# Optimization experiments

Hardware: AMD Instinct MI355X
Metric: run time of the kernel (lower is better)

Reference implementation:

```python
import jax, jax.numpy as jnp
import numpy as np

N_NODES = 100000
N_EDGES = 1000000
N_GRAPHS = 1024
F_IN = 128
N_CLASSES = 10
BN_EPS = 1e-5


def _lin(key, fan_in, fan_out):
    k1, k2 = jax.random.split(key)
    b = 1.0 / np.sqrt(fan_in)
    W = jax.random.uniform(k1, (fan_out, fan_in), minval=-b, maxval=b, dtype=jnp.float32)
    bias = jax.random.uniform(k2, (fan_out,), minval=-b, maxval=b, dtype=jnp.float32)
    return W, bias


def setup_inputs() -> dict:
    key = jax.random.key(0)
    ks = jax.random.split(key, 16)
    inp = {
        "atom_feats": jax.random.normal(ks[0], (N_NODES, F_IN), dtype=jnp.float32),
        "edge_src": jax.random.randint(ks[1], (N_EDGES,), 0, N_NODES),
        "edge_dst": jax.random.randint(ks[2], (N_EDGES,), 0, N_NODES),
        "graph_ids": jnp.sort(jax.random.randint(ks[3], (N_NODES,), 0, N_GRAPHS)),
    }
    # conv1: F_IN -> 32 with batch-norm on edge features
    inp["Wt1"], inp["bt1"] = _lin(ks[4], F_IN, 32)
    inp["Wp1"], inp["bp1"] = _lin(ks[5], F_IN, 32)
    inp["bn_gamma"] = jnp.ones((32,), jnp.float32)
    inp["bn_beta"] = jnp.zeros((32,), jnp.float32)
    inp["bn_mean"] = jnp.zeros((32,), jnp.float32)
    inp["bn_var"] = jnp.ones((32,), jnp.float32)
    # conv2: 32 -> 64 ; conv3: 64 -> 64
    inp["Wt2"], inp["bt2"] = _lin(ks[6], 32, 64)
    inp["Wp2"], inp["bp2"] = _lin(ks[7], 32, 64)
    inp["Wt3"], inp["bt3"] = _lin(ks[8], 64, 64)
    inp["Wp3"], inp["bp3"] = _lin(ks[9], 64, 64)
    # fc layers
    inp["Wf1"], inp["bf1"] = _lin(ks[10], 64, 64)
    inp["Wf2"], inp["bf2"] = _lin(ks[11], 64, 32)
    inp["Wf3"], inp["bf3"] = _lin(ks[12], 32, N_CLASSES)
    return inp


def _seg_max(vals, ids, n):
    m = jax.ops.segment_max(vals, ids, num_segments=n)
    return jnp.where(jnp.isfinite(m), m, 0.0)  # zero-in-degree -> 0 (DGL semantics)


def _edgeconv(x, src, dst, Wt, bt, Wp, bp, bn=None):
    xs = x[src]                      # [E, f_in] gather src
    xd = x[dst]                      # [E, f_in] gather dst
    e = (xd - xs) @ Wt.T + bt + (xs @ Wp.T + bp)  # [E, f_out]
    if bn is not None:
        gamma, beta, mean, var = bn
        e = (e - mean) * (gamma / jnp.sqrt(var + BN_EPS)) + beta
    return _seg_max(e, dst, x.shape[0])


def reference(atom_feats, edge_src, edge_dst, graph_ids,
              Wt1, bt1, Wp1, bp1, bn_gamma, bn_beta, bn_mean, bn_var,
              Wt2, bt2, Wp2, bp2, Wt3, bt3, Wp3, bp3,
              Wf1, bf1, Wf2, bf2, Wf3, bf3):
    x = jax.nn.elu(_edgeconv(atom_feats, edge_src, edge_dst, Wt1, bt1, Wp1, bp1,
                             bn=(bn_gamma, bn_beta, bn_mean, bn_var)))
    x = jax.nn.elu(_edgeconv(x, edge_src, edge_dst, Wt2, bt2, Wp2, bp2))
    x = jax.nn.elu(_edgeconv(x, edge_src, edge_dst, Wt3, bt3, Wp3, bp3))
    x = _seg_max(x, graph_ids, N_GRAPHS)          # graph-level max pooling [G, 64]
    x = jax.nn.elu(x @ Wf1.T + bf1)               # dropout is identity in eval mode
    x = jax.nn.elu(x @ Wf2.T + bf2)
    x = x @ Wf3.T + bf3
    return jax.nn.log_softmax(x, axis=1)
```

## Files before the change

kernel.cpp:

```cpp
#include <hip/hip_runtime.h>
#include <hip/hip_fp16.h>
#include <math.h>

#define N_NODES 100000
#define N_EDGES 1000000
#define N_GRAPHS 1024
#define BN_EPS 1e-5f

#define BUCKET_NODES 128
#define NB_BUCKETS ((N_NODES + BUCKET_NODES - 1) / BUCKET_NODES)
#define BUCKET_PAD 2048
#define BUCKET_CAP 3072
#define SCAT_CHUNK 2048

typedef __attribute__((__ext_vector_type__(8))) _Float16 f16x8;
typedef __attribute__((__ext_vector_type__(4))) _Float16 f16x4;
typedef __attribute__((__ext_vector_type__(4))) float f32x4;

static __device__ __forceinline__ float elu_f(float v) {
    return v > 0.f ? v : expm1f(v);
}

static __device__ __forceinline__ unsigned pkmax(unsigned a, unsigned b) {
    unsigned r;
    asm("v_pk_max_f16 %0, %1, %2" : "=v"(r) : "v"(a), "v"(b));
    return r;
}
#define HALF2_NEG_INF 0xFC00FC00u

static __device__ __forceinline__ uint4 pkmax4(uint4 a, uint4 b) {
    uint4 r;
    r.x = pkmax(a.x, b.x);
    r.y = pkmax(a.y, b.y);
    r.z = pkmax(a.z, b.z);
    r.w = pkmax(a.w, b.w);
    return r;
}

static __device__ __forceinline__ unsigned fmap(float f) {
    unsigned u = __float_as_uint(f);
    return (u & 0x80000000u) ? ~u : (u | 0x80000000u);
}
static __device__ __forceinline__ float funmap(unsigned u) {
    unsigned b = (u & 0x80000000u) ? (u & 0x7FFFFFFFu) : ~u;
    return __uint_as_float(b);
}
#define NEG_INF_MAPPED 0x007FFFFFu

__global__ __launch_bounds__(256) void prep_kernel(
        const float* __restrict__ Wt1, const float* __restrict__ bt1,
        const float* __restrict__ Wp1, const float* __restrict__ bp1,
        const float* __restrict__ gamma, const float* __restrict__ beta,
        const float* __restrict__ mean,  const float* __restrict__ var,
        const float* __restrict__ Wt2, const float* __restrict__ bt2,
        const float* __restrict__ Wp2, const float* __restrict__ bp2,
        const float* __restrict__ Wt3, const float* __restrict__ bt3,
        const float* __restrict__ Wp3, const float* __restrict__ bp3,
        __half* __restrict__ wsz1, float* __restrict__ qb1,
        __half* __restrict__ wsz2, float* __restrict__ qb2,
        __half* __restrict__ wsz3, float* __restrict__ qb3,
        int* __restrict__ cursor, unsigned* __restrict__ pooled) {
    int idx = blockIdx.x * 256 + threadIdx.x;

    if (idx < NB_BUCKETS) cursor[idx] = 0;
    for (int j = idx; j < N_GRAPHS * 64; j += 8192) pooled[j] = NEG_INF_MAPPED;

    {
        const int K = 128, F = 32, NCF = 4;
        if (idx < K * 2 * F) {
            int frag = idx >> 9, within = idx & 511, lane = within >> 3, j = within & 7;
            int kf = frag / NCF, cf = frag % NCF;
            int k = kf * 32 + (lane >> 4) * 8 + j;
            int c = cf * 16 + (lane & 15);
            float v;
            if (c < F) {
                float s = gamma[c] * rsqrtf(var[c] + BN_EPS);
                v = Wt1[c * K + k] * s;
            } else {
                int cc = c - F;
                float s = gamma[cc] * rsqrtf(var[cc] + BN_EPS);
                v = (Wp1[cc * K + k] - Wt1[cc * K + k]) * s;
            }
            wsz1[idx] = __float2half(v);
        }
        if (idx < F) {
            float s = gamma[idx] * rsqrtf(var[idx] + BN_EPS);
            qb1[idx] = (bt1[idx] + bp1[idx]) * s + beta[idx] - mean[idx] * s;
        }
    }
    {
        const int K = 32, F = 64, NCF = 8;
        if (idx < K * 2 * F) {
            int frag = idx >> 9, within = idx & 511, lane = within >> 3, j = within & 7;
            int kf = frag / NCF, cf = frag % NCF;
            int k = kf * 32 + (lane >> 4) * 8 + j;
            int c = cf * 16 + (lane & 15);
            float v = (c < F) ? Wt2[c * K + k]
                              : (Wp2[(c - F) * K + k] - Wt2[(c - F) * K + k]);
            wsz2[idx] = __float2half(v);
        }
        if (idx < F) qb2[idx] = bt2[idx] + bp2[idx];
    }
    {
        const int K = 64, F = 64, NCF = 8;
        if (idx < K * 2 * F) {
            int frag = idx >> 9, within = idx & 511, lane = within >> 3, j = within & 7;
            int kf = frag / NCF, cf = frag % NCF;
            int k = kf * 32 + (lane >> 4) * 8 + j;
            int c = cf * 16 + (lane & 15);
            float v = (c < F) ? Wt3[c * K + k]
                              : (Wp3[(c - F) * K + k] - Wt3[(c - F) * K + k]);
            wsz3[idx] = __float2half(v);
        }
        if (idx < F) qb3[idx] = bt3[idx] + bp3[idx];
    }
}

__global__ __launch_bounds__(256) void scatter_kernel(const int* __restrict__ esrc,
                                                      const int* __restrict__ edst,
                                                      int* __restrict__ cursor,
                                                      unsigned* __restrict__ binned, int E) {
    __shared__ int hist[NB_BUCKETS];
    __shared__ int lbase[NB_BUCKETS];
    __shared__ unsigned pk[SCAT_CHUNK];
    __shared__ unsigned short bk[SCAT_CHUNK];
    int begE = blockIdx.x * SCAT_CHUNK;
    int endE = min(begE + SCAT_CHUNK, E);
    int n = endE - begE;
    for (int i = threadIdx.x; i < NB_BUCKETS; i += 256) hist[i] = 0;
    __syncthreads();
    for (int i = threadIdx.x; i < n; i += 256) {
        int d = edst[begE + i];
        int s = esrc[begE + i];
        int b = d >> 7;
        pk[i] = ((unsigned)s << 7) | (unsigned)(d & 127);
        bk[i] = (unsigned short)b;
        atomicAdd(&hist[b], 1);
    }
    __syncthreads();
    for (int i = threadIdx.x; i < NB_BUCKETS; i += 256) {
        int c = hist[i];
        lbase[i] = c ? (i * BUCKET_PAD + atomicAdd(&cursor[i], c)) : 0;
        hist[i] = 0;
    }
    __syncthreads();
    for (int i = threadIdx.x; i < n; i += 256) {
        int b = bk[i];
        int pos = lbase[b] + atomicAdd(&hist[b], 1);
        binned[pos] = pk[i];
    }
}

__global__ __launch_bounds__(256) void bucket_build_kernel(const unsigned* __restrict__ binned,
                                                           const int* __restrict__ bcount,
                                                           int* __restrict__ begs,
                                                           int* __restrict__ ends,
                                                           int* __restrict__ csr) {
    __shared__ unsigned stage[BUCKET_CAP];
    __shared__ int srcLDS[BUCKET_CAP];
    __shared__ int cnt[BUCKET_NODES];
    __shared__ int sc[BUCKET_NODES];
    __shared__ int loff[BUCKET_NODES];

    int b = blockIdx.x;
    int ebeg = b * BUCKET_PAD;
    int ne = min(bcount[b], BUCKET_CAP);
    int tid = threadIdx.x;

    if (tid < BUCKET_NODES) cnt[tid] = 0;
    __syncthreads();
    for (int i = tid; i < ne; i += 256) {
        unsigned e = binned[ebeg + i];
        stage[i] = e;
        atomicAdd(&cnt[e & 127], 1);
    }
    __syncthreads();
    int v = (tid < BUCKET_NODES) ? cnt[tid] : 0;
    if (tid < BUCKET_NODES) sc[tid] = v;
    __syncthreads();
    for (int off = 1; off < BUCKET_NODES; off <<= 1) {
        int u = (tid < BUCKET_NODES && tid >= off) ? sc[tid - off] : 0;
        __syncthreads();
        if (tid < BUCKET_NODES) sc[tid] += u;
        __syncthreads();
    }
    if (tid < BUCKET_NODES) {
        loff[tid] = sc[tid] - v;
        cnt[tid] = 0;
    }
    __syncthreads();
    int gnode = b * BUCKET_NODES + tid;
    if (tid < BUCKET_NODES && gnode < N_NODES) {
        begs[gnode] = ebeg + loff[tid];
        ends[gnode] = ebeg + loff[tid] + v;
    }
    for (int i = tid; i < ne; i += 256) {
        unsigned e = stage[i];
        int ln = e & 127;
        int slot = loff[ln] + atomicAdd(&cnt[ln], 1);
        srcLDS[slot] = (int)(e >> 7);
    }
    __syncthreads();
    for (int i = tid; i < ne; i += 256) csr[ebeg + i] = srcLDS[i];
}

template <int K>
static __device__ __forceinline__ f16x8 load_xfrag(const __half* __restrict__ x,
                                                   size_t rowIdx, int kOff) {
    return *reinterpret_cast<const f16x8*>(x + rowIdx * K + kOff);
}
template <int K>
static __device__ __forceinline__ f16x8 load_xfrag(const float* __restrict__ x,
                                                   size_t rowIdx, int kOff) {
    const float* xr = x + rowIdx * K + kOff;
    float4 a0 = *reinterpret_cast<const float4*>(xr);
    float4 a1 = *reinterpret_cast<const float4*>(xr + 4);
    f16x8 a;
    a[0] = (_Float16)a0.x; a[1] = (_Float16)a0.y; a[2] = (_Float16)a0.z; a[3] = (_Float16)a0.w;
    a[4] = (_Float16)a1.x; a[5] = (_Float16)a1.y; a[6] = (_Float16)a1.z; a[7] = (_Float16)a1.w;
    return a;
}

template <int K, int F, typename IT>
__global__ __launch_bounds__(256) void transform_mfma(
        const IT* __restrict__ x, const __half* __restrict__ wsz,
        const float* __restrict__ qb,
        __half* __restrict__ t, __half* __restrict__ q) {
    constexpr int NKF = K / 32;
    constexpr int NCF = (2 * F) / 16;
    constexpr int NTILES = N_NODES / 16;

    int lane = threadIdx.x & 63;
    int wid = blockIdx.x * 4 + (threadIdx.x >> 6);
    int nWaves = gridDim.x * 4;

    f16x8 wfrag[NKF][NCF];
#pragma unroll
    for (int kf = 0; kf < NKF; kf++)
#pragma unroll
        for (int cf = 0; cf < NCF; cf++)
            wfrag[kf][cf] = *reinterpret_cast<const f16x8*>(
                wsz + ((size_t)(kf * NCF + cf) * 64 + lane) * 8);

    int nrow = lane & 15;
    int kq8 = (lane >> 4) * 8;
    int c4 = (lane >> 4) * 4;

    for (int tile = wid; tile < NTILES; tile += nWaves) {
        size_t nodeBase = (size_t)tile * 16;

        f32x4 acc[NCF];
#pragma unroll
        for (int cf = 0; cf < NCF; cf++) acc[cf] = (f32x4){0.f, 0.f, 0.f, 0.f};

#pragma unroll
        for (int kf = 0; kf < NKF; kf++) {
            f16x8 a = load_xfrag<K>(x, nodeBase + nrow, kf * 32 + kq8);
#pragma unroll
            for (int cf = 0; cf < NCF; cf++)
                acc[cf] = __builtin_amdgcn_mfma_f32_16x16x32_f16(wfrag[kf][cf], a, acc[cf], 0, 0, 0);
        }

        size_t node = nodeBase + nrow;
#pragma unroll
        for (int cf = 0; cf < NCF; cf++) {
            int c = cf * 16 + c4;
            if (c < F) {
                f16x4 h;
#pragma unroll
                for (int r = 0; r < 4; r++) h[r] = (_Float16)acc[cf][r];
                *reinterpret_cast<f16x4*>(t + node * F + c) = h;
            } else {
                float4 qv = *reinterpret_cast<const float4*>(qb + (c - F));
                f16x4 h;
                h[0] = (_Float16)(acc[cf][0] + qv.x);
                h[1] = (_Float16)(acc[cf][1] + qv.y);
                h[2] = (_Float16)(acc[cf][2] + qv.z);
                h[3] = (_Float16)(acc[cf][3] + qv.w);
                *reinterpret_cast<f16x4*>(q + node * F + (c - F)) = h;
            }
        }
    }
}

template <int F>
__global__ __launch_bounds__(256) void edgemax_kernel(
        const uint4* __restrict__ t16, const uint4* __restrict__ q16,
        const int* __restrict__ begs, const int* __restrict__ ends,
        const int* __restrict__ csr,
        uint4* __restrict__ out, int N) {
    constexpr int NPG = F / 8;
    constexpr int G = 256 / NPG;
    int g = threadIdx.x / NPG;
    int cp = threadIdx.x % NPG;
    int nd = blockIdx.x * G + g;
    if (nd >= N) return;
    int beg = begs[nd], end = ends[nd];

    uint4 mneg = {HALF2_NEG_INF, HALF2_NEG_INF, HALF2_NEG_INF, HALF2_NEG_INF};
    uint4 m0 = mneg, m1 = mneg, m2 = mneg, m3 = mneg;
    int i = beg;
    for (; i + 3 < end; i += 4) {
        int s0 = csr[i], s1 = csr[i + 1], s2 = csr[i + 2], s3 = csr[i + 3];
        uint4 v0 = q16[(size_t)s0 * NPG + cp];
        uint4 v1 = q16[(size_t)s1 * NPG + cp];
        uint4 v2 = q16[(size_t)s2 * NPG + cp];
        uint4 v3 = q16[(size_t)s3 * NPG + cp];
        m0 = pkmax4(m0, v0);
        m1 = pkmax4(m1, v1);
        m2 = pkmax4(m2, v2);
        m3 = pkmax4(m3, v3);
    }
    for (; i < end; i++) {
        m0 = pkmax4(m0, q16[(size_t)csr[i] * NPG + cp]);
    }
    uint4 m = pkmax4(pkmax4(m0, m1), pkmax4(m2, m3));

    uint4 res;
    if (beg < end) {
        uint4 tv = t16[(size_t)nd * NPG + cp];
        unsigned* mp = &m.x;
        unsigned* tp = &tv.x;
        unsigned* rp = &res.x;
#pragma unroll
        for (int w = 0; w < 4; w++) {
            float2 mf = __half22float2(__builtin_bit_cast(__half2, mp[w]));
            float2 tf = __half22float2(__builtin_bit_cast(__half2, tp[w]));
            float rx = elu_f(tf.x + mf.x);
            float ry = elu_f(tf.y + mf.y);
            rp[w] = __builtin_bit_cast(unsigned, __floats2half2_rn(rx, ry));
        }
    } else {
        res = (uint4){0u, 0u, 0u, 0u};
    }
    out[(size_t)nd * NPG + cp] = res;
}

__global__ void pool_kernel(const __half* __restrict__ x, const int* __restrict__ gid,
                            unsigned* __restrict__ pooled, int N) {
    const int CHUNK = 64;
    int wave = (blockIdx.x * blockDim.x + threadIdx.x) >> 6;
    int lane = threadIdx.x & 63;
    int start = wave * CHUNK;
    if (start >= N) return;
    int end = min(start + CHUNK, N);
    float m = -INFINITY;
    int cur = gid[start];
    for (int n = start; n < end; n++) {
        int g = gid[n];
        if (g != cur) {
            atomicMax(&pooled[cur * 64 + lane], fmap(m));
            cur = g;
            m = -INFINITY;
        }
        m = fmaxf(m, __half2float(x[(size_t)n * 64 + lane]));
    }
    atomicMax(&pooled[cur * 64 + lane], fmap(m));
}

__global__ __launch_bounds__(64) void fc_kernel(
        const unsigned* __restrict__ pooled,
        const float* __restrict__ Wf1, const float* __restrict__ bf1,
        const float* __restrict__ Wf2, const float* __restrict__ bf2,
        const float* __restrict__ Wf3, const float* __restrict__ bf3,
        float* __restrict__ out) {
    int g = blockIdx.x;
    int c = threadIdx.x;
    __shared__ float x0[64], h1[64], h2[32], h3[10];

    unsigned u = pooled[g * 64 + c];
    x0[c] = (u == NEG_INF_MAPPED) ? 0.f : funmap(u);
    __syncthreads();

    float a = bf1[c];
#pragma unroll 8
    for (int k = 0; k < 64; k++) a = fmaf(Wf1[c * 64 + k], x0[k], a);
    h1[c] = elu_f(a);
    __syncthreads();

    if (c < 32) {
        float a2 = bf2[c];
#pragma unroll 8
        for (int k = 0; k < 64; k++) a2 = fmaf(Wf2[c * 64 + k], h1[k], a2);
        h2[c] = elu_f(a2);
    }
    __syncthreads();

    if (c < 10) {
        float a3 = bf3[c];
#pragma unroll 8
        for (int k = 0; k < 32; k++) a3 = fmaf(Wf3[c * 32 + k], h2[k], a3);
        h3[c] = a3;
    }
    __syncthreads();

    if (c < 10) {
        float mx = h3[0];
#pragma unroll
        for (int j = 1; j < 10; j++) mx = fmaxf(mx, h3[j]);
        float s = 0.f;
#pragma unroll
        for (int j = 0; j < 10; j++) s += expf(h3[j] - mx);
        out[g * 10 + c] = h3[c] - mx - logf(s);
    }
}

extern "C" void kernel_launch(void* const* d_in, const int* in_sizes, int n_in,
                              void* d_out, int out_size, void* d_ws, size_t ws_size,
                              hipStream_t stream) {
    const float* atom = (const float*)d_in[0];
    const int* esrc = (const int*)d_in[1];
    const int* edst = (const int*)d_in[2];
    const int* gid  = (const int*)d_in[3];
    const float* Wt1 = (const float*)d_in[4];
    const float* bt1 = (const float*)d_in[5];
    const float* Wp1 = (const float*)d_in[6];
    const float* bp1 = (const float*)d_in[7];
    const float* bng = (const float*)d_in[8];
    const float* bnb = (const float*)d_in[9];
    const float* bnm = (const float*)d_in[10];
    const float* bnv = (const float*)d_in[11];
    const float* Wt2 = (const float*)d_in[12];
    const float* bt2 = (const float*)d_in[13];
    const float* Wp2 = (const float*)d_in[14];
    const float* bp2 = (const float*)d_in[15];
    const float* Wt3 = (const float*)d_in[16];
    const float* bt3 = (const float*)d_in[17];
    const float* Wp3 = (const float*)d_in[18];
    const float* bp3 = (const float*)d_in[19];
    const float* Wf1 = (const float*)d_in[20];
    const float* bf1 = (const float*)d_in[21];
    const float* Wf2 = (const float*)d_in[22];
    const float* bf2 = (const float*)d_in[23];
    const float* Wf3 = (const float*)d_in[24];
    const float* bf3 = (const float*)d_in[25];

    char* p = (char*)d_ws;
    auto alloc = [&](size_t bytes) -> void* {
        void* r = (void*)p;
        p += (bytes + 255) & ~(size_t)255;
        return r;
    };
    int* begs        = (int*)alloc(sizeof(int) * N_NODES);
    int* ends        = (int*)alloc(sizeof(int) * N_NODES);
    int* cursor      = (int*)alloc(sizeof(int) * NB_BUCKETS);
    unsigned* binned = (unsigned*)alloc(sizeof(unsigned) * NB_BUCKETS * BUCKET_PAD);
    int* csr         = (int*)alloc(sizeof(int) * NB_BUCKETS * BUCKET_PAD);
    __half* wsz1 = (__half*)alloc(sizeof(__half) * 128 * 64);
    __half* wsz2 = (__half*)alloc(sizeof(__half) * 32 * 128);
    __half* wsz3 = (__half*)alloc(sizeof(__half) * 64 * 128);
    float* qb1   = (float*)alloc(sizeof(float) * 32);
    float* qb2   = (float*)alloc(sizeof(float) * 64);
    float* qb3   = (float*)alloc(sizeof(float) * 64);
    __half* tbuf = (__half*)alloc(sizeof(__half) * (size_t)N_NODES * 64);
    __half* qbuf = (__half*)alloc(sizeof(__half) * (size_t)N_NODES * 64);
    __half* xh   = (__half*)alloc(sizeof(__half) * (size_t)N_NODES * 64);
    unsigned* pooled = (unsigned*)alloc(sizeof(unsigned) * N_GRAPHS * 64);

    prep_kernel<<<32, 256, 0, stream>>>(Wt1, bt1, Wp1, bp1, bng, bnb, bnm, bnv,
                                        Wt2, bt2, Wp2, bp2, Wt3, bt3, Wp3, bp3,
                                        wsz1, qb1, wsz2, qb2, wsz3, qb3, cursor, pooled);
    scatter_kernel<<<(N_EDGES + SCAT_CHUNK - 1) / SCAT_CHUNK, 256, 0, stream>>>(
        esrc, edst, cursor, binned, N_EDGES);
    bucket_build_kernel<<<NB_BUCKETS, 256, 0, stream>>>(binned, cursor, begs, ends, csr);

    transform_mfma<128, 32, float><<<782, 256, 0, stream>>>(atom, wsz1, qb1, tbuf, qbuf);
    edgemax_kernel<32><<<(N_NODES + 63) / 64, 256, 0, stream>>>(
        (const uint4*)tbuf, (const uint4*)qbuf, begs, ends, csr, (uint4*)xh, N_NODES);

    transform_mfma<32, 64, __half><<<782, 256, 0, stream>>>(xh, wsz2, qb2, tbuf, qbuf);
    edgemax_kernel<64><<<(N_NODES + 31) / 32, 256, 0, stream>>>(
        (const uint4*)tbuf, (const uint4*)qbuf, begs, ends, csr, (uint4*)xh, N_NODES);

    transform_mfma<64, 64, __half><<<782, 256, 0, stream>>>(xh, wsz3, qb3, tbuf, qbuf);
    edgemax_kernel<64><<<(N_NODES + 31) / 32, 256, 0, stream>>>(
        (const uint4*)tbuf, (const uint4*)qbuf, begs, ends, csr, (uint4*)xh, N_NODES);

    {
        int waves = (N_NODES + 63) / 64;
        int blocks = (waves + 3) / 4;
        pool_kernel<<<blocks, 256, 0, stream>>>(xh, gid, pooled, N_NODES);
    }

    fc_kernel<<<N_GRAPHS, 64, 0, stream>>>(pooled, Wf1, bf1, Wf2, bf2, Wf3, bf3, (float*)d_out);
}
```

Before: 182.0 us.

## Store node features in 8-channel slice-major layout for sliced edge-max gathers

Node feature buffers (t, q, x) are switched from row-major [N, F] to a slice-major layout [F/8][N][8], and the transform, edge-max and pooling kernels are updated to match. Edge-max now gives each thread one node and one 16-byte channel slice, and blocks are ordered so the slices for the same node chunk run close together. The goal is for each gathered slice array to be small enough to stay resident in cache, which would improve hit rates for the random neighbor gathers. The cost is that each thread now re-reads the CSR indices once per slice, and transform stores become strided across slices.

```diff
diff --git a/kernel.cpp b/kernel.cpp
--- a/kernel.cpp
+++ b/kernel.cpp
@@ -206,13 +206,13 @@
 
 template <int K>
 static __device__ __forceinline__ f16x8 load_xfrag(const __half* __restrict__ x,
-                                                   size_t rowIdx, int kOff) {
-    return *reinterpret_cast<const f16x8*>(x + rowIdx * K + kOff);
+                                                   size_t node, int kOff) {
+    return *reinterpret_cast<const f16x8*>(x + ((size_t)(kOff >> 3) * N_NODES + node) * 8);
 }
 template <int K>
 static __device__ __forceinline__ f16x8 load_xfrag(const float* __restrict__ x,
-                                                   size_t rowIdx, int kOff) {
-    const float* xr = x + rowIdx * K + kOff;
+                                                   size_t node, int kOff) {
+    const float* xr = x + node * K + kOff;
     float4 a0 = *reinterpret_cast<const float4*>(xr);
     float4 a1 = *reinterpret_cast<const float4*>(xr + 4);
     f16x8 a;
@@ -269,32 +269,38 @@
                 f16x4 h;
 #pragma unroll
                 for (int r = 0; r < 4; r++) h[r] = (_Float16)acc[cf][r];
-                *reinterpret_cast<f16x4*>(t + node * F + c) = h;
+                *reinterpret_cast<f16x4*>(t + ((size_t)(c >> 3) * N_NODES + node) * 8 + (c & 7)) = h;
             } else {
-                float4 qv = *reinterpret_cast<const float4*>(qb + (c - F));
+                int cc = c - F;
+                float4 qv = *reinterpret_cast<const float4*>(qb + cc);
                 f16x4 h;
                 h[0] = (_Float16)(acc[cf][0] + qv.x);
                 h[1] = (_Float16)(acc[cf][1] + qv.y);
                 h[2] = (_Float16)(acc[cf][2] + qv.z);
                 h[3] = (_Float16)(acc[cf][3] + qv.w);
-                *reinterpret_cast<f16x4*>(q + node * F + (c - F)) = h;
+                *reinterpret_cast<f16x4*>(q + ((size_t)(cc >> 3) * N_NODES + node) * 8 + (cc & 7)) = h;
             }
         }
     }
 }
 
 template <int F>
-__global__ __launch_bounds__(256) void edgemax_kernel(
-        const uint4* __restrict__ t16, const uint4* __restrict__ q16,
+__global__ __launch_bounds__(256) void edgemax_slice_kernel(
+        const uint4* __restrict__ ts,
+        const uint4* __restrict__ qs,
         const int* __restrict__ begs, const int* __restrict__ ends,
         const int* __restrict__ csr,
-        uint4* __restrict__ out, int N) {
-    constexpr int NPG = F / 8;
-    constexpr int G = 256 / NPG;
-    int g = threadIdx.x / NPG;
-    int cp = threadIdx.x % NPG;
-    int nd = blockIdx.x * G + g;
+        uint4* __restrict__ outs, int N) {
+    constexpr int NSLICE = F / 8;
+    constexpr int REP = 8 / NSLICE;
+    int vs = blockIdx.x & 7;
+    int slice = vs / REP;
+    int sub = vs % REP;
+    int chunk = (blockIdx.x >> 3) * REP + sub;
+    int nd = chunk * 256 + threadIdx.x;
     if (nd >= N) return;
+
+    const uint4* q = qs + (size_t)slice * N;
     int beg = begs[nd], end = ends[nd];
 
     uint4 mneg = {HALF2_NEG_INF, HALF2_NEG_INF, HALF2_NEG_INF, HALF2_NEG_INF};
@@ -302,23 +308,17 @@
     int i = beg;
     for (; i + 3 < end; i += 4) {
         int s0 = csr[i], s1 = csr[i + 1], s2 = csr[i + 2], s3 = csr[i + 3];
-        uint4 v0 = q16[(size_t)s0 * NPG + cp];
-        uint4 v1 = q16[(size_t)s1 * NPG + cp];
-        uint4 v2 = q16[(size_t)s2 * NPG + cp];
-        uint4 v3 = q16[(size_t)s3 * NPG + cp];
-        m0 = pkmax4(m0, v0);
-        m1 = pkmax4(m1, v1);
-        m2 = pkmax4(m2, v2);
-        m3 = pkmax4(m3, v3);
-    }
-    for (; i < end; i++) {
-        m0 = pkmax4(m0, q16[(size_t)csr[i] * NPG + cp]);
-    }
+        m0 = pkmax4(m0, q[s0]);
+        m1 = pkmax4(m1, q[s1]);
+        m2 = pkmax4(m2, q[s2]);
+        m3 = pkmax4(m3, q[s3]);
+    }
+    for (; i < end; i++) m0 = pkmax4(m0, q[csr[i]]);
     uint4 m = pkmax4(pkmax4(m0, m1), pkmax4(m2, m3));
 
     uint4 res;
     if (beg < end) {
-        uint4 tv = t16[(size_t)nd * NPG + cp];
+        uint4 tv = ts[(size_t)slice * N + nd];
         unsigned* mp = &m.x;
         unsigned* tp = &tv.x;
         unsigned* rp = &res.x;
@@ -333,7 +333,7 @@
     } else {
         res = (uint4){0u, 0u, 0u, 0u};
     }
-    out[(size_t)nd * NPG + cp] = res;
+    outs[(size_t)slice * N + nd] = res;
 }
 
 __global__ void pool_kernel(const __half* __restrict__ x, const int* __restrict__ gid,
@@ -344,6 +344,7 @@
     int start = wave * CHUNK;
     if (start >= N) return;
     int end = min(start + CHUNK, N);
+    const __half* base = x + (size_t)(lane >> 3) * N_NODES * 8 + (lane & 7);
     float m = -INFINITY;
     int cur = gid[start];
     for (int n = start; n < end; n++) {
@@ -353,7 +354,7 @@
             cur = g;
             m = -INFINITY;
         }
-        m = fmaxf(m, __half2float(x[(size_t)n * 64 + lane]));
+        m = fmaxf(m, __half2float(base[(size_t)n * 8]));
     }
     atomicMax(&pooled[cur * 64 + lane], fmap(m));
 }
@@ -457,6 +458,8 @@
     __half* xh   = (__half*)alloc(sizeof(__half) * (size_t)N_NODES * 64);
     unsigned* pooled = (unsigned*)alloc(sizeof(unsigned) * N_GRAPHS * 64);
 
+    const int NCHUNK = (N_NODES + 255) / 256;
+
     prep_kernel<<<32, 256, 0, stream>>>(Wt1, bt1, Wp1, bp1, bng, bnb, bnm, bnv,
                                         Wt2, bt2, Wp2, bp2, Wt3, bt3, Wp3, bp3,
                                         wsz1, qb1, wsz2, qb2, wsz3, qb3, cursor, pooled);
@@ -465,15 +468,15 @@
     bucket_build_kernel<<<NB_BUCKETS, 256, 0, stream>>>(binned, cursor, begs, ends, csr);
 
     transform_mfma<128, 32, float><<<782, 256, 0, stream>>>(atom, wsz1, qb1, tbuf, qbuf);
-    edgemax_kernel<32><<<(N_NODES + 63) / 64, 256, 0, stream>>>(
+    edgemax_slice_kernel<32><<<8 * ((NCHUNK + 1) / 2), 256, 0, stream>>>(
         (const uint4*)tbuf, (const uint4*)qbuf, begs, ends, csr, (uint4*)xh, N_NODES);
 
     transform_mfma<32, 64, __half><<<782, 256, 0, stream>>>(xh, wsz2, qb2, tbuf, qbuf);
-    edgemax_kernel<64><<<(N_NODES + 31) / 32, 256, 0, stream>>>(
+    edgemax_slice_kernel<64><<<8 * NCHUNK, 256, 0, stream>>>(
         (const uint4*)tbuf, (const uint4*)qbuf, begs, ends, csr, (uint4*)xh, N_NODES);
 
     transform_mfma<64, 64, __half><<<782, 256, 0, stream>>>(xh, wsz3, qb3, tbuf, qbuf);
-    edgemax_kernel<64><<<(N_NODES + 31) / 32, 256, 0, stream>>>(
+    edgemax_slice_kernel<64><<<8 * NCHUNK, 256, 0, stream>>>(
         (const uint4*)tbuf, (const uint4*)qbuf, begs, ends, csr, (uint4*)xh, N_NODES);
 
     {
```

Result: slower. 220.3 us (+21.1%).

## Sort nodes by in-degree within buckets to balance edgemax wavefronts

Applied to the files above, without the earlier changes.

The bucket build kernel now counting-sorts each bucket's 128 nodes by in-degree (capped at 63) and writes a per-bucket rank-to-node permutation. The edgemax kernels iterate over ranks and look up node ids through this permutation, so threads in the same wavefront handle nodes with similar degree and loop divergence drops. The cost is an extra indirection load, a larger grid padded to whole buckets, and a serial single-thread prefix scan inside bucket build.

```diff
diff --git a/kernel.cpp b/kernel.cpp
--- a/kernel.cpp
+++ b/kernel.cpp
@@ -12,6 +12,7 @@
 #define BUCKET_PAD 2048
 #define BUCKET_CAP 3072
 #define SCAT_CHUNK 2048
+#define N_RANKS (NB_BUCKETS * BUCKET_NODES)
 
 typedef __attribute__((__ext_vector_type__(8))) _Float16 f16x8;
 typedef __attribute__((__ext_vector_type__(4))) _Float16 f16x4;
@@ -59,11 +60,13 @@
         __half* __restrict__ wsz1, float* __restrict__ qb1,
         __half* __restrict__ wsz2, float* __restrict__ qb2,
         __half* __restrict__ wsz3, float* __restrict__ qb3,
-        int* __restrict__ cursor, unsigned* __restrict__ pooled) {
+        int* __restrict__ cursor, unsigned* __restrict__ pooled,
+        int* __restrict__ ord) {
     int idx = blockIdx.x * 256 + threadIdx.x;
 
     if (idx < NB_BUCKETS) cursor[idx] = 0;
     for (int j = idx; j < N_GRAPHS * 64; j += 8192) pooled[j] = NEG_INF_MAPPED;
+    for (int j = idx; j < N_RANKS; j += 8192) ord[j] = N_NODES;
 
     {
         const int K = 128, F = 32, NCF = 4;
@@ -155,12 +158,15 @@
                                                            const int* __restrict__ bcount,
                                                            int* __restrict__ begs,
                                                            int* __restrict__ ends,
-                                                           int* __restrict__ csr) {
+                                                           int* __restrict__ csr,
+                                                           int* __restrict__ ord) {
     __shared__ unsigned stage[BUCKET_CAP];
     __shared__ int srcLDS[BUCKET_CAP];
     __shared__ int cnt[BUCKET_NODES];
     __shared__ int sc[BUCKET_NODES];
     __shared__ int loff[BUCKET_NODES];
+    __shared__ int dhist[64];
+    __shared__ int dcur[64];
 
     int b = blockIdx.x;
     int ebeg = b * BUCKET_PAD;
@@ -168,6 +174,7 @@
     int tid = threadIdx.x;
 
     if (tid < BUCKET_NODES) cnt[tid] = 0;
+    if (tid < 64) { dhist[tid] = 0; dcur[tid] = 0; }
     __syncthreads();
     for (int i = tid; i < ne; i += 256) {
         unsigned e = binned[ebeg + i];
@@ -190,9 +197,22 @@
     }
     __syncthreads();
     int gnode = b * BUCKET_NODES + tid;
-    if (tid < BUCKET_NODES && gnode < N_NODES) {
+    bool validNode = (tid < BUCKET_NODES) && (gnode < N_NODES);
+    if (validNode) {
         begs[gnode] = ebeg + loff[tid];
         ends[gnode] = ebeg + loff[tid] + v;
+    }
+    int bin = min(v, 63);
+    if (validNode) atomicAdd(&dhist[bin], 1);
+    __syncthreads();
+    if (tid == 0) {
+        int run = 0;
+        for (int i = 0; i < 64; i++) { int c = dhist[i]; dhist[i] = run; run += c; }
+    }
+    __syncthreads();
+    if (validNode) {
+        int r = dhist[bin] + atomicAdd(&dcur[bin], 1);
+        ord[b * BUCKET_NODES + r] = gnode;
     }
     for (int i = tid; i < ne; i += 256) {
         unsigned e = stage[i];
@@ -206,13 +226,13 @@
 
 template <int K>
 static __device__ __forceinline__ f16x8 load_xfrag(const __half* __restrict__ x,
-                                                   size_t rowIdx, int kOff) {
-    return *reinterpret_cast<const f16x8*>(x + rowIdx * K + kOff);
+                                                   size_t node, int kOff) {
+    return *reinterpret_cast<const f16x8*>(x + node * K + kOff);
 }
 template <int K>
 static __device__ __forceinline__ f16x8 load_xfrag(const float* __restrict__ x,
-                                                   size_t rowIdx, int kOff) {
-    const float* xr = x + rowIdx * K + kOff;
+                                                   size_t node, int kOff) {
+    const float* xr = x + node * K + kOff;
     float4 a0 = *reinterpret_cast<const float4*>(xr);
     float4 a1 = *reinterpret_cast<const float4*>(xr + 4);
     f16x8 a;
@@ -271,13 +291,14 @@
                 for (int r = 0; r < 4; r++) h[r] = (_Float16)acc[cf][r];
                 *reinterpret_cast<f16x4*>(t + node * F + c) = h;
             } else {
-                float4 qv = *reinterpret_cast<const float4*>(qb + (c - F));
+                int cc = c - F;
+                float4 qv = *reinterpret_cast<const float4*>(qb + cc);
                 f16x4 h;
                 h[0] = (_Float16)(acc[cf][0] + qv.x);
                 h[1] = (_Float16)(acc[cf][1] + qv.y);
                 h[2] = (_Float16)(acc[cf][2] + qv.z);
                 h[3] = (_Float16)(acc[cf][3] + qv.w);
-                *reinterpret_cast<f16x4*>(q + node * F + (c - F)) = h;
+                *reinterpret_cast<f16x4*>(q + node * F + cc) = h;
             }
         }
     }
@@ -287,13 +308,14 @@
 __global__ __launch_bounds__(256) void edgemax_kernel(
         const uint4* __restrict__ t16, const uint4* __restrict__ q16,
         const int* __restrict__ begs, const int* __restrict__ ends,
-        const int* __restrict__ csr,
+        const int* __restrict__ csr, const int* __restrict__ ord,
         uint4* __restrict__ out, int N) {
     constexpr int NPG = F / 8;
     constexpr int G = 256 / NPG;
     int g = threadIdx.x / NPG;
     int cp = threadIdx.x % NPG;
-    int nd = blockIdx.x * G + g;
+    int rank = blockIdx.x * G + g;
+    int nd = ord[rank];
     if (nd >= N) return;
     int beg = begs[nd], end = ends[nd];
 
@@ -302,14 +324,10 @@
     int i = beg;
     for (; i + 3 < end; i += 4) {
         int s0 = csr[i], s1 = csr[i + 1], s2 = csr[i + 2], s3 = csr[i + 3];
-        uint4 v0 = q16[(size_t)s0 * NPG + cp];
-        uint4 v1 = q16[(size_t)s1 * NPG + cp];
-        uint4 v2 = q16[(size_t)s2 * NPG + cp];
-        uint4 v3 = q16[(size_t)s3 * NPG + cp];
-        m0 = pkmax4(m0, v0);
-        m1 = pkmax4(m1, v1);
-        m2 = pkmax4(m2, v2);
-        m3 = pkmax4(m3, v3);
+        m0 = pkmax4(m0, q16[(size_t)s0 * NPG + cp]);
+        m1 = pkmax4(m1, q16[(size_t)s1 * NPG + cp]);
+        m2 = pkmax4(m2, q16[(size_t)s2 * NPG + cp]);
+        m3 = pkmax4(m3, q16[(size_t)s3 * NPG + cp]);
     }
     for (; i < end; i++) {
         m0 = pkmax4(m0, q16[(size_t)csr[i] * NPG + cp]);
@@ -443,6 +461,7 @@
     };
     int* begs        = (int*)alloc(sizeof(int) * N_NODES);
     int* ends        = (int*)alloc(sizeof(int) * N_NODES);
+    int* ord         = (int*)alloc(sizeof(int) * N_RANKS);
     int* cursor      = (int*)alloc(sizeof(int) * NB_BUCKETS);
     unsigned* binned = (unsigned*)alloc(sizeof(unsigned) * NB_BUCKETS * BUCKET_PAD);
     int* csr         = (int*)alloc(sizeof(int) * NB_BUCKETS * BUCKET_PAD);
@@ -459,22 +478,22 @@
 
     prep_kernel<<<32, 256, 0, stream>>>(Wt1, bt1, Wp1, bp1, bng, bnb, bnm, bnv,
                                         Wt2, bt2, Wp2, bp2, Wt3, bt3, Wp3, bp3,
-                                        wsz1, qb1, wsz2, qb2, wsz3, qb3, cursor, pooled);
+                                        wsz1, qb1, wsz2, qb2, wsz3, qb3, cursor, pooled, ord);
     scatter_kernel<<<(N_EDGES + SCAT_CHUNK - 1) / SCAT_CHUNK, 256, 0, stream>>>(
         esrc, edst, cursor, binned, N_EDGES);
-    bucket_build_kernel<<<NB_BUCKETS, 256, 0, stream>>>(binned, cursor, begs, ends, csr);
+    bucket_build_kernel<<<NB_BUCKETS, 256, 0, stream>>>(binned, cursor, begs, ends, csr, ord);
 
     transform_mfma<128, 32, float><<<782, 256, 0, stream>>>(atom, wsz1, qb1, tbuf, qbuf);
-    edgemax_kernel<32><<<(N_NODES + 63) / 64, 256, 0, stream>>>(
-        (const uint4*)tbuf, (const uint4*)qbuf, begs, ends, csr, (uint4*)xh, N_NODES);
+    edgemax_kernel<32><<<N_RANKS / 64, 256, 0, stream>>>(
+        (const uint4*)tbuf, (const uint4*)qbuf, begs, ends, csr, ord, (uint4*)xh, N_NODES);
 
     transform_mfma<32, 64, __half><<<782, 256, 0, stream>>>(xh, wsz2, qb2, tbuf, qbuf);
-    edgemax_kernel<64><<<(N_NODES + 31) / 32, 256, 0, stream>>>(
-        (const uint4*)tbuf, (const uint4*)qbuf, begs, ends, csr, (uint4*)xh, N_NODES);
+    edgemax_kernel<64><<<N_RANKS / 32, 256, 0, stream>>>(
+        (const uint4*)tbuf, (const uint4*)qbuf, begs, ends, csr, ord, (uint4*)xh, N_NODES);
 
     transform_mfma<64, 64, __half><<<782, 256, 0, stream>>>(xh, wsz3, qb3, tbuf, qbuf);
-    edgemax_kernel<64><<<(N_NODES + 31) / 32, 256, 0, stream>>>(
-        (const uint4*)tbuf, (const uint4*)qbuf, begs, ends, csr, (uint4*)xh, N_NODES);
+    edgemax_kernel<64><<<N_RANKS / 32, 256, 0, stream>>>(
+        (const uint4*)tbuf, (const uint4*)qbuf, begs, ends, csr, ord, (uint4*)xh, N_NODES);
 
     {
         int waves = (N_NODES + 63) / 64;
```

Result: slower. 190.9 us (+4.9%).
